# Kernel tuning notes

Hardware: AMD Instinct MI355X
Metric: run time of the kernel (lower is better)

Reference implementation:

```python
import jax, jax.numpy as jnp
import numpy as np

M, NQ, NKV = 8, 256, 4096
E, H, D = 1024, 16, 64  # embed_dim, num_heads, head_dim
SCALE = D ** -0.5


def setup_inputs() -> dict:
    key = jax.random.key(0)
    ks = jax.random.split(key, 6)
    zq = jax.random.normal(ks[0], (M, NQ, E), dtype=jnp.float32)
    zkv = jax.random.normal(ks[1], (M, NKV, E), dtype=jnp.float32)
    xq = jax.random.normal(ks[2], (M, NQ, E), dtype=jnp.float32)
    xkv = jax.random.normal(ks[3], (M, NKV, E), dtype=jnp.float32)
    Wq = jax.random.normal(ks[4], (E, H * D), dtype=jnp.float32) / np.sqrt(E)
    Wk = jax.random.normal(ks[5], (E, H * D), dtype=jnp.float32) / np.sqrt(E)
    raw_head_weights = jnp.ones((H,), dtype=jnp.float32)
    return {"zq": zq, "zkv": zkv, "xq": xq, "xkv": xkv,
            "Wq": Wq, "Wk": Wk, "raw_head_weights": raw_head_weights}


def reference(zq, zkv, xq, xkv, Wq, Wk, raw_head_weights):
    # project + split heads: [m, h, n, d]
    q = jnp.einsum('mne,ehd->mhnd', zq, Wq.reshape(E, H, D))
    k = jnp.einsum('mne,ehd->mhnd', zkv, Wk.reshape(E, H, D))
    # SDPA with V = xkv broadcast across heads
    scores = jnp.einsum('mhqd,mhkd->mhqk', q, k) * SCALE
    attn = jax.nn.softmax(scores, axis=-1)
    # attn @ V with broadcast V [m, nkv, dx] -> per-head outputs [m, h, nq, dx]
    out = jnp.einsum('mhqk,mkd->mhqd', attn, xkv)
    # head-weighted combine + residual
    head_weights = jax.nn.softmax(raw_head_weights, axis=0)
    xq_update = jnp.einsum('mhqd,h->mqd', out, head_weights)
    xq_out = xq + xq_update
    return (zq, xq_out)
```

## Files before the change

### kernel.cpp

```cpp
#include <hip/hip_runtime.h>
#include <hip/hip_bf16.h>
#include <stdint.h>

#define MB_  8
#define NQ_  256
#define NKV_ 4096
#define E_   1024
#define H_   16
#define D_   64

typedef __bf16 bf16x8 __attribute__((ext_vector_type(8)));
typedef float  f32x4  __attribute__((ext_vector_type(4)));
typedef unsigned short u16;
typedef unsigned short u16x8 __attribute__((ext_vector_type(8)));

#define MFMA16(a,b,c) __builtin_amdgcn_mfma_f32_16x16x32_bf16((a),(b),(c),0,0,0)

__device__ __forceinline__ u16 f2bf(float f) {
  uint32_t u = __float_as_uint(f);
  u += 0x7fffu + ((u >> 16) & 1u);
  return (u16)(u >> 16);
}

__device__ __forceinline__ void gload_lds16(const void* g, void* l) {
  __builtin_amdgcn_global_load_lds(
      (const __attribute__((address_space(1))) void*)g,
      (__attribute__((address_space(3))) void*)l, 16, 0, 0);
}

__device__ __forceinline__ void stage_tile(const char* __restrict__ g, int ldbytes,
                                           char* lds, int t) {
  int srcCB = (((t & 7) ^ ((t >> 3) & 7)) << 4);
  const char* gp = g + (long long)(t >> 3) * ldbytes + srcCB;
  char* lp = lds + ((t >> 6) << 10);
#pragma unroll
  for (int i = 0; i < 4; ++i) {
    gload_lds16(gp + (long long)(32 * i) * ldbytes, lp + i * 4096);
  }
}

__device__ __forceinline__ bf16x8 read_frag(const char* lds, int r, int cb) {
  return *(const bf16x8*)(lds + r * 128 + (cb ^ ((r & 7) << 4)));
}

template <int MODE>
__global__ __launch_bounds__(256, 2) void gemm_nt(
    const u16* __restrict__ A, const u16* __restrict__ Bt, void* __restrict__ Cv,
    const float* __restrict__ resid,
    int lda, int ldb, int ldc, int K,
    long long sA, long long sB, long long sC, long long sR) {
  __shared__ __align__(16) char smA[16384];
  __shared__ __align__(16) char smB[16384];
  int b = blockIdx.z;
  unsigned nwg = gridDim.x * gridDim.y;
  unsigned orig = blockIdx.y * gridDim.x + blockIdx.x;
  unsigned cpx = nwg >> 3;
  unsigned swz = (orig & 7) * cpx + (orig >> 3);
  unsigned bx = swz % gridDim.x, by = swz / gridDim.x;

  const char* Ap = (const char*)(A + (long long)b * sA + (long long)by * 128 * lda);
  const char* Bp = (const char*)(Bt + (long long)b * sB + (long long)bx * 128 * ldb);
  int t = threadIdx.x, lane = t & 63;
  int wm = t >> 7, wn = (t >> 6) & 1;
  int rl = lane & 15, kq = lane >> 4;

  f32x4 acc[4][4];
#pragma unroll
  for (int i = 0; i < 4; ++i)
#pragma unroll
    for (int j = 0; j < 4; ++j) acc[i][j] = (f32x4){0.f, 0.f, 0.f, 0.f};

  int ldab = lda * 2, ldbb = ldb * 2;
  for (int k0 = 0; k0 < K; k0 += 64) {
    stage_tile(Ap + k0 * 2, ldab, smA, t);
    stage_tile(Bp + k0 * 2, ldbb, smB, t);
    __syncthreads();
    bf16x8 af[4][2], bf[4][2];
#pragma unroll
    for (int f = 0; f < 4; ++f)
#pragma unroll
      for (int ks = 0; ks < 2; ++ks) {
        af[f][ks] = read_frag(smA, wm * 64 + f * 16 + rl, ks * 64 + kq * 16);
        bf[f][ks] = read_frag(smB, wn * 64 + f * 16 + rl, ks * 64 + kq * 16);
      }
#pragma unroll
    for (int fm = 0; fm < 4; ++fm)
#pragma unroll
      for (int fn = 0; fn < 4; ++fn) {
        acc[fm][fn] = MFMA16(af[fm][0], bf[fn][0], acc[fm][fn]);
        acc[fm][fn] = MFMA16(af[fm][1], bf[fn][1], acc[fm][fn]);
      }
    __syncthreads();
  }

#pragma unroll
  for (int fm = 0; fm < 4; ++fm)
#pragma unroll
    for (int fn = 0; fn < 4; ++fn)
#pragma unroll
      for (int j = 0; j < 4; ++j) {
        int row = by * 128 + wm * 64 + fm * 16 + kq * 4 + j;
        int col = bx * 128 + wn * 64 + fn * 16 + rl;
        long long o = (long long)b * sC + (long long)row * ldc + col;
        if (MODE == 0) {
          ((u16*)Cv)[o] = f2bf(acc[fm][fn][j]);
        } else {
          ((float*)Cv)[o] =
              resid[(long long)b * sR + (long long)row * ldc + col] + acc[fm][fn][j];
        }
      }
}

__global__ __launch_bounds__(256, 4) void attn_stats(
    const u16* __restrict__ qg, const u16* __restrict__ kg,
    float* __restrict__ lstP) {
  __shared__ __align__(16) char smQ[16384];
  __shared__ __align__(16) char smK[16384];
  int kt = blockIdx.x, qt = blockIdx.y;
  int m = blockIdx.z >> 1, hh = blockIdx.z & 1;
  int t = threadIdx.x, lane = t & 63;
  int wm = t >> 7, wn = (t >> 6) & 1;
  int rl = lane & 15, kq = lane >> 4;

  const char* qbase = (const char*)(qg + ((long long)(m * NQ_ + qt * 128)) * 1024);
  const char* kbase = (const char*)(kg + ((long long)(m * NKV_ + kt * 128)) * 1024);

  for (int hi = 0; hi < 8; ++hi) {
    int h = hh * 8 + hi;
    stage_tile(qbase + h * 128, 2048, smQ, t);
    stage_tile(kbase + h * 128, 2048, smK, t);
    __syncthreads();
    bf16x8 kf[4][2], qf[4][2];
#pragma unroll
    for (int f = 0; f < 4; ++f)
#pragma unroll
      for (int ks = 0; ks < 2; ++ks) {
        kf[f][ks] = read_frag(smK, wm * 64 + f * 16 + rl, ks * 64 + kq * 16);
        qf[f][ks] = read_frag(smQ, wn * 64 + f * 16 + rl, ks * 64 + kq * 16);
      }
    float rs[4] = {0.f, 0.f, 0.f, 0.f};
#pragma unroll
    for (int fm = 0; fm < 4; ++fm)
#pragma unroll
      for (int fn = 0; fn < 4; ++fn) {
        f32x4 sc = (f32x4){0.f, 0.f, 0.f, 0.f};
        sc = MFMA16(kf[fm][0], qf[fn][0], sc);
        sc = MFMA16(kf[fm][1], qf[fn][1], sc);
        rs[fn] += (__expf(sc[0]) + __expf(sc[1])) + (__expf(sc[2]) + __expf(sc[3]));
      }
#pragma unroll
    for (int fn = 0; fn < 4; ++fn) {
      float v = rs[fn];
      v += __shfl_xor(v, 16);
      v += __shfl_xor(v, 32);
      if (lane < 16) {
        int q = qt * 128 + wn * 64 + fn * 16 + rl;
        lstP[(long long)(kt * 2 + wm) * 32768 + ((m * H_ + h) << 8) + q] = v;
      }
    }
    __syncthreads();
  }
}

__global__ void stats_combine(const float* __restrict__ lp, float* __restrict__ lst) {
  int i = blockIdx.x * 256 + threadIdx.x;
  float s = 0.f;
#pragma unroll
  for (int k = 0; k < 64; ++k) s += lp[(long long)k * 32768 + i];
  lst[i] = s;
}

__global__ __launch_bounds__(256, 2) void pbar_kernel(
    const u16* __restrict__ qg, const u16* __restrict__ kg,
    const float* __restrict__ lstat,
    const float* __restrict__ rawhw, u16* __restrict__ Pbar) {
  __shared__ __align__(16) char smQ[16384];
  __shared__ __align__(16) char smK[16384];
  __shared__ float scf[2048];
  int kt = blockIdx.x, qt = blockIdx.y, m = blockIdx.z;
  int q0 = qt * 128, k0 = kt * 128;
  int t = threadIdx.x, lane = t & 63;
  int wm = t >> 7, wn = (t >> 6) & 1;
  int rl = lane & 15, kq = lane >> 4;

  float hm = -1e30f;
  for (int i = 0; i < H_; ++i) hm = fmaxf(hm, rawhw[i]);
  float hs = 0.f, hw[H_];
  for (int i = 0; i < H_; ++i) { hw[i] = __expf(rawhw[i] - hm); hs += hw[i]; }
  float hinv = 1.f / hs;
  for (int idx = t; idx < 2048; idx += 256) {
    int h = idx >> 7, r = idx & 127;
    scf[idx] = hw[h] * hinv / lstat[((m * H_ + h) << 8) + q0 + r];
  }

  f32x4 pacc[4][4];
#pragma unroll
  for (int i = 0; i < 4; ++i)
#pragma unroll
    for (int j = 0; j < 4; ++j) pacc[i][j] = (f32x4){0.f, 0.f, 0.f, 0.f};

  const char* qbase = (const char*)(qg + ((long long)(m * NQ_ + q0)) * 1024);
  const char* kbase = (const char*)(kg + ((long long)(m * NKV_ + k0)) * 1024);

  for (int h = 0; h < H_; ++h) {
    stage_tile(qbase + h * 128, 2048, smQ, t);
    stage_tile(kbase + h * 128, 2048, smK, t);
    __syncthreads();
    bf16x8 af[4][2], bfr[4][2];
#pragma unroll
    for (int f = 0; f < 4; ++f)
#pragma unroll
      for (int ks = 0; ks < 2; ++ks) {
        af[f][ks] = read_frag(smQ, wm * 64 + f * 16 + rl, ks * 64 + kq * 16);
        bfr[f][ks] = read_frag(smK, wn * 64 + f * 16 + rl, ks * 64 + kq * 16);
      }
#pragma unroll
    for (int fm = 0; fm < 4; ++fm) {
      int rbase = wm * 64 + fm * 16 + kq * 4;
      float cf0 = scf[(h << 7) + rbase + 0];
      float cf1 = scf[(h << 7) + rbase + 1];
      float cf2 = scf[(h << 7) + rbase + 2];
      float cf3 = scf[(h << 7) + rbase + 3];
#pragma unroll
      for (int fn = 0; fn < 4; ++fn) {
        f32x4 sc = (f32x4){0.f, 0.f, 0.f, 0.f};
        sc = MFMA16(af[fm][0], bfr[fn][0], sc);
        sc = MFMA16(af[fm][1], bfr[fn][1], sc);
        pacc[fm][fn][0] += cf0 * __expf(sc[0]);
        pacc[fm][fn][1] += cf1 * __expf(sc[1]);
        pacc[fm][fn][2] += cf2 * __expf(sc[2]);
        pacc[fm][fn][3] += cf3 * __expf(sc[3]);
      }
    }
    __syncthreads();
  }
#pragma unroll
  for (int fm = 0; fm < 4; ++fm)
#pragma unroll
    for (int fn = 0; fn < 4; ++fn)
#pragma unroll
      for (int j = 0; j < 4; ++j) {
        int row = q0 + wm * 64 + fm * 16 + kq * 4 + j;
        int col = k0 + wn * 64 + fn * 16 + rl;
        Pbar[(((long long)m * NQ_ + row) << 12) + col] = f2bf(pacc[fm][fn][j]);
      }
}

__global__ void cvt8(const float* __restrict__ in, u16* __restrict__ out, long long n8) {
  long long i = (long long)blockIdx.x * 256 + threadIdx.x;
  if (i >= n8) return;
  const float4* p = (const float4*)in + i * 2;
  float4 a = p[0], b = p[1];
  u16x8 v;
  v[0] = f2bf(a.x); v[1] = f2bf(a.y); v[2] = f2bf(a.z); v[3] = f2bf(a.w);
  v[4] = f2bf(b.x); v[5] = f2bf(b.y); v[6] = f2bf(b.z); v[7] = f2bf(b.w);
  *(u16x8*)(out + i * 8) = v;
}

__global__ void tcvt(const float* __restrict__ in, u16* __restrict__ out,
                     int R, int C, long long sIn, long long sOut, float alpha) {
  __shared__ float tile[32][33];
  long long bIn = (long long)blockIdx.z * sIn;
  long long bOut = (long long)blockIdx.z * sOut;
  int c0 = blockIdx.x * 32, r0 = blockIdx.y * 32;
  int tx = threadIdx.x, ty = threadIdx.y;
#pragma unroll
  for (int i = 0; i < 32; i += 8)
    tile[ty + i][tx] = in[bIn + (long long)(r0 + ty + i) * C + c0 + tx];
  __syncthreads();
#pragma unroll
  for (int i = 0; i < 32; i += 8)
    out[bOut + (long long)(c0 + ty + i) * R + r0 + tx] = f2bf(alpha * tile[tx][ty + i]);
}

extern "C" void kernel_launch(void* const* d_in, const int* in_sizes, int n_in,
                              void* d_out, int out_size, void* d_ws, size_t ws_size,
                              hipStream_t stream) {
  const float* zq  = (const float*)d_in[0];
  const float* zkv = (const float*)d_in[1];
  const float* xq  = (const float*)d_in[2];
  const float* xkv = (const float*)d_in[3];
  const float* Wq  = (const float*)d_in[4];
  const float* Wk  = (const float*)d_in[5];
  const float* rhw = (const float*)d_in[6];
  float* out = (float*)d_out;

  char* ws = (char*)d_ws;
  u16* WqT  = (u16*)(ws);
  u16* WkT  = (u16*)(ws + (2ull << 20));
  u16* zqb  = (u16*)(ws + (4ull << 20));
  u16* qb   = (u16*)(ws + (8ull << 20));
  u16* kb   = (u16*)(ws + (12ull << 20));
  u16* xkvT = (u16*)(ws + (76ull << 20));
  char* zr  = ws + (140ull << 20);
  u16* zkvb = (u16*)zr;
  u16* Pbar = (u16*)zr;
  float* lst  = (float*)(zr + (18ull << 20));
  float* lstP = (float*)(zr + (20ull << 20));

  hipMemcpyAsync(d_out, (const void*)zq, (size_t)MB_ * NQ_ * E_ * sizeof(float),
                 hipMemcpyDeviceToDevice, stream);

  cvt8<<<(MB_ * NQ_ * E_) / 8 / 256, 256, 0, stream>>>(zq, zqb, (MB_ * NQ_ * E_) / 8);
  cvt8<<<(MB_ * NKV_ * E_) / 8 / 256, 256, 0, stream>>>(zkv, zkvb, (long long)(MB_ * NKV_ * E_) / 8);
  dim3 tb(32, 8);
  tcvt<<<dim3(32, 32, 1), tb, 0, stream>>>(Wq, WqT, 1024, 1024, 0, 0, 0.125f);
  tcvt<<<dim3(32, 32, 1), tb, 0, stream>>>(Wk, WkT, 1024, 1024, 0, 0, 1.0f);
  tcvt<<<dim3(32, 128, 8), tb, 0, stream>>>(xkv, xkvT, NKV_, E_,
                                            (long long)NKV_ * E_, (long long)NKV_ * E_, 1.0f);

  gemm_nt<0><<<dim3(8, 16, 1), 256, 0, stream>>>(zqb, WqT, qb, nullptr,
                                                 1024, 1024, 1024, 1024, 0, 0, 0, 0);
  gemm_nt<0><<<dim3(8, 256, 1), 256, 0, stream>>>(zkvb, WkT, kb, nullptr,
                                                  1024, 1024, 1024, 1024, 0, 0, 0, 0);

  attn_stats<<<dim3(32, 2, 16), 256, 0, stream>>>(qb, kb, lstP);
  stats_combine<<<128, 256, 0, stream>>>(lstP, lst);

  pbar_kernel<<<dim3(32, 2, 8), 256, 0, stream>>>(qb, kb, lst, rhw, Pbar);

  gemm_nt<1><<<dim3(8, 2, 8), 256, 0, stream>>>(Pbar, xkvT, out + (long long)MB_ * NQ_ * E_, xq,
                                                4096, 4096, 1024, 4096,
                                                256LL * 4096, 1024LL * 4096,
                                                256LL * 1024, 256LL * 1024);
}
```

Baseline: 351.5 us.

## Fuse fp32-to-bf16 conversion into projection GEMMs and split-K the PV GEMM

The separate cvt8 passes over zq and zkv are removed. The projection GEMMs now load fp32 tiles directly and convert them to bf16 while writing to LDS, which saves a full write and read of the 64MB bf16 zkv copy. The PV GEMM, which previously ran only 128 blocks over K=4096, is split into 4 K-chunks (512 blocks) that write fp32 partials. A new combine kernel sums the partials and adds the xq residual. The tradeoff is that A-tile staging in the projections no longer uses async global_load_lds, and the split adds partial-buffer traffic plus one extra kernel launch.

```diff
diff --git a/kernel.cpp b/kernel.cpp
--- a/kernel.cpp
+++ b/kernel.cpp
@@ -39,27 +39,51 @@
   }
 }
 
+__device__ __forceinline__ void stage_tile_f32(const float* __restrict__ g, int ldf,
+                                               char* lds, int t) {
+#pragma unroll
+  for (int i = 0; i < 8; ++i) {
+    int flat = t + i * 256;
+    int row = flat >> 4;
+    int c4 = flat & 15;
+    float4 v = *(const float4*)(g + (long long)row * ldf + c4 * 4);
+    uint32_t lo = (uint32_t)f2bf(v.x) | ((uint32_t)f2bf(v.y) << 16);
+    uint32_t hi = (uint32_t)f2bf(v.z) | ((uint32_t)f2bf(v.w) << 16);
+    int cb = (c4 * 8) ^ ((row & 7) << 4);
+    *(uint2*)(lds + row * 128 + cb) = make_uint2(lo, hi);
+  }
+}
+
 __device__ __forceinline__ bf16x8 read_frag(const char* lds, int r, int cb) {
   return *(const bf16x8*)(lds + r * 128 + (cb ^ ((r & 7) << 4)));
 }
 
-template <int MODE>
+template <int MODE, int ASRC>
 __global__ __launch_bounds__(256, 2) void gemm_nt(
-    const u16* __restrict__ A, const u16* __restrict__ Bt, void* __restrict__ Cv,
-    const float* __restrict__ resid,
+    const void* __restrict__ Av, const u16* __restrict__ Bt, void* __restrict__ Cv,
     int lda, int ldb, int ldc, int K,
-    long long sA, long long sB, long long sC, long long sR) {
+    long long sA, long long sB, long long sC) {
   __shared__ __align__(16) char smA[16384];
   __shared__ __align__(16) char smB[16384];
-  int b = blockIdx.z;
+  int zz = blockIdx.z;
+  int b = (MODE == 2) ? (zz & 7) : zz;
+  int ks = (MODE == 2) ? (zz >> 3) : 0;
+  long long koff = (long long)ks * 1024;
+
   unsigned nwg = gridDim.x * gridDim.y;
   unsigned orig = blockIdx.y * gridDim.x + blockIdx.x;
   unsigned cpx = nwg >> 3;
   unsigned swz = (orig & 7) * cpx + (orig >> 3);
   unsigned bx = swz % gridDim.x, by = swz / gridDim.x;
 
-  const char* Ap = (const char*)(A + (long long)b * sA + (long long)by * 128 * lda);
-  const char* Bp = (const char*)(Bt + (long long)b * sB + (long long)bx * 128 * ldb);
+  const char* Ap;
+  const float* Apf;
+  if (ASRC == 0)
+    Ap = (const char*)((const u16*)Av + (long long)b * sA + (long long)by * 128 * lda + koff);
+  else
+    Apf = (const float*)Av + (long long)b * sA + (long long)by * 128 * lda + koff;
+  const char* Bp = (const char*)(Bt + (long long)b * sB + (long long)bx * 128 * ldb + koff);
+
   int t = threadIdx.x, lane = t & 63;
   int wm = t >> 7, wn = (t >> 6) & 1;
   int rl = lane & 15, kq = lane >> 4;
@@ -72,16 +96,19 @@
 
   int ldab = lda * 2, ldbb = ldb * 2;
   for (int k0 = 0; k0 < K; k0 += 64) {
-    stage_tile(Ap + k0 * 2, ldab, smA, t);
+    if (ASRC == 0)
+      stage_tile(Ap + k0 * 2, ldab, smA, t);
+    else
+      stage_tile_f32(Apf + k0, lda, smA, t);
     stage_tile(Bp + k0 * 2, ldbb, smB, t);
     __syncthreads();
     bf16x8 af[4][2], bf[4][2];
 #pragma unroll
     for (int f = 0; f < 4; ++f)
 #pragma unroll
-      for (int ks = 0; ks < 2; ++ks) {
-        af[f][ks] = read_frag(smA, wm * 64 + f * 16 + rl, ks * 64 + kq * 16);
-        bf[f][ks] = read_frag(smB, wn * 64 + f * 16 + rl, ks * 64 + kq * 16);
+      for (int ksl = 0; ksl < 2; ++ksl) {
+        af[f][ksl] = read_frag(smA, wm * 64 + f * 16 + rl, ksl * 64 + kq * 16);
+        bf[f][ksl] = read_frag(smB, wn * 64 + f * 16 + rl, ksl * 64 + kq * 16);
       }
 #pragma unroll
     for (int fm = 0; fm < 4; ++fm)
@@ -101,14 +128,25 @@
       for (int j = 0; j < 4; ++j) {
         int row = by * 128 + wm * 64 + fm * 16 + kq * 4 + j;
         int col = bx * 128 + wn * 64 + fn * 16 + rl;
-        long long o = (long long)b * sC + (long long)row * ldc + col;
         if (MODE == 0) {
-          ((u16*)Cv)[o] = f2bf(acc[fm][fn][j]);
+          ((u16*)Cv)[(long long)b * sC + (long long)row * ldc + col] = f2bf(acc[fm][fn][j]);
         } else {
-          ((float*)Cv)[o] =
-              resid[(long long)b * sR + (long long)row * ldc + col] + acc[fm][fn][j];
+          ((float*)Cv)[((long long)(ks * 8 + b)) * sC + (long long)row * ldc + col] =
+              acc[fm][fn][j];
         }
       }
+}
+
+__global__ void pv_combine(const float* __restrict__ part, const float* __restrict__ xq,
+                           float* __restrict__ out) {
+  int i = blockIdx.x * 256 + threadIdx.x;
+  float4 s = ((const float4*)xq)[i];
+#pragma unroll
+  for (int k = 0; k < 4; ++k) {
+    float4 p = ((const float4*)(part + (long long)k * 2097152))[i];
+    s.x += p.x; s.y += p.y; s.z += p.z; s.w += p.w;
+  }
+  ((float4*)out)[i] = s;
 }
 
 __global__ __launch_bounds__(256, 4) void attn_stats(
@@ -134,9 +172,9 @@
 #pragma unroll
     for (int f = 0; f < 4; ++f)
 #pragma unroll
-      for (int ks = 0; ks < 2; ++ks) {
-        kf[f][ks] = read_frag(smK, wm * 64 + f * 16 + rl, ks * 64 + kq * 16);
-        qf[f][ks] = read_frag(smQ, wn * 64 + f * 16 + rl, ks * 64 + kq * 16);
+      for (int ksl = 0; ksl < 2; ++ksl) {
+        kf[f][ksl] = read_frag(smK, wm * 64 + f * 16 + rl, ksl * 64 + kq * 16);
+        qf[f][ksl] = read_frag(smQ, wn * 64 + f * 16 + rl, ksl * 64 + kq * 16);
       }
     float rs[4] = {0.f, 0.f, 0.f, 0.f};
 #pragma unroll
@@ -210,9 +248,9 @@
 #pragma unroll
     for (int f = 0; f < 4; ++f)
 #pragma unroll
-      for (int ks = 0; ks < 2; ++ks) {
-        af[f][ks] = read_frag(smQ, wm * 64 + f * 16 + rl, ks * 64 + kq * 16);
-        bfr[f][ks] = read_frag(smK, wn * 64 + f * 16 + rl, ks * 64 + kq * 16);
+      for (int ksl = 0; ksl < 2; ++ksl) {
+        af[f][ksl] = read_frag(smQ, wm * 64 + f * 16 + rl, ksl * 64 + kq * 16);
+        bfr[f][ksl] = read_frag(smK, wn * 64 + f * 16 + rl, ksl * 64 + kq * 16);
       }
 #pragma unroll
     for (int fm = 0; fm < 4; ++fm) {
@@ -244,17 +282,6 @@
         int col = k0 + wn * 64 + fn * 16 + rl;
         Pbar[(((long long)m * NQ_ + row) << 12) + col] = f2bf(pacc[fm][fn][j]);
       }
-}
-
-__global__ void cvt8(const float* __restrict__ in, u16* __restrict__ out, long long n8) {
-  long long i = (long long)blockIdx.x * 256 + threadIdx.x;
-  if (i >= n8) return;
-  const float4* p = (const float4*)in + i * 2;
-  float4 a = p[0], b = p[1];
-  u16x8 v;
-  v[0] = f2bf(a.x); v[1] = f2bf(a.y); v[2] = f2bf(a.z); v[3] = f2bf(a.w);
-  v[4] = f2bf(b.x); v[5] = f2bf(b.y); v[6] = f2bf(b.z); v[7] = f2bf(b.w);
-  *(u16x8*)(out + i * 8) = v;
 }
 
 __global__ void tcvt(const float* __restrict__ in, u16* __restrict__ out,
@@ -288,39 +315,37 @@
   char* ws = (char*)d_ws;
   u16* WqT  = (u16*)(ws);
   u16* WkT  = (u16*)(ws + (2ull << 20));
-  u16* zqb  = (u16*)(ws + (4ull << 20));
   u16* qb   = (u16*)(ws + (8ull << 20));
   u16* kb   = (u16*)(ws + (12ull << 20));
   u16* xkvT = (u16*)(ws + (76ull << 20));
   char* zr  = ws + (140ull << 20);
-  u16* zkvb = (u16*)zr;
   u16* Pbar = (u16*)zr;
   float* lst  = (float*)(zr + (18ull << 20));
   float* lstP = (float*)(zr + (20ull << 20));
+  float* pvP  = (float*)(zr + (28ull << 20));
 
   hipMemcpyAsync(d_out, (const void*)zq, (size_t)MB_ * NQ_ * E_ * sizeof(float),
                  hipMemcpyDeviceToDevice, stream);
 
-  cvt8<<<(MB_ * NQ_ * E_) / 8 / 256, 256, 0, stream>>>(zq, zqb, (MB_ * NQ_ * E_) / 8);
-  cvt8<<<(MB_ * NKV_ * E_) / 8 / 256, 256, 0, stream>>>(zkv, zkvb, (long long)(MB_ * NKV_ * E_) / 8);
   dim3 tb(32, 8);
   tcvt<<<dim3(32, 32, 1), tb, 0, stream>>>(Wq, WqT, 1024, 1024, 0, 0, 0.125f);
   tcvt<<<dim3(32, 32, 1), tb, 0, stream>>>(Wk, WkT, 1024, 1024, 0, 0, 1.0f);
   tcvt<<<dim3(32, 128, 8), tb, 0, stream>>>(xkv, xkvT, NKV_, E_,
                                             (long long)NKV_ * E_, (long long)NKV_ * E_, 1.0f);
 
-  gemm_nt<0><<<dim3(8, 16, 1), 256, 0, stream>>>(zqb, WqT, qb, nullptr,
-                                                 1024, 1024, 1024, 1024, 0, 0, 0, 0);
-  gemm_nt<0><<<dim3(8, 256, 1), 256, 0, stream>>>(zkvb, WkT, kb, nullptr,
-                                                  1024, 1024, 1024, 1024, 0, 0, 0, 0);
+  gemm_nt<0, 1><<<dim3(8, 16, 1), 256, 0, stream>>>(zq, WqT, qb,
+                                                    1024, 1024, 1024, 1024, 0, 0, 0);
+  gemm_nt<0, 1><<<dim3(8, 256, 1), 256, 0, stream>>>(zkv, WkT, kb,
+                                                     1024, 1024, 1024, 1024, 0, 0, 0);
 
   attn_stats<<<dim3(32, 2, 16), 256, 0, stream>>>(qb, kb, lstP);
   stats_combine<<<128, 256, 0, stream>>>(lstP, lst);
 
   pbar_kernel<<<dim3(32, 2, 8), 256, 0, stream>>>(qb, kb, lst, rhw, Pbar);
 
-  gemm_nt<1><<<dim3(8, 2, 8), 256, 0, stream>>>(Pbar, xkvT, out + (long long)MB_ * NQ_ * E_, xq,
-                                                4096, 4096, 1024, 4096,
-                                                256LL * 4096, 1024LL * 4096,
-                                                256LL * 1024, 256LL * 1024);
-}
+  gemm_nt<2, 0><<<dim3(8, 2, 32), 256, 0, stream>>>(Pbar, xkvT, pvP,
+                                                    4096, 4096, 1024, 1024,
+                                                    256LL * 4096, 1024LL * 4096,
+                                                    256LL * 1024);
+  pv_combine<<<2048, 256, 0, stream>>>(pvP, xq, out + (long long)MB_ * NQ_ * E_);
+}
```

New measurement: 497.2 us. +41.4%, slower.
